# Kernel tuning notes

Hardware: AMD Instinct MI355X
Metric: run time of the kernel (lower is better)

The kernel has to match this reference:

```python
import jax, jax.numpy as jnp
import numpy as np


def setup_inputs() -> dict:
    key = jax.random.key(0)
    k1, k2 = jax.random.split(key)
    N, C, H, W = 2, 128, 256, 256
    k, m = 7, 8
    feat = jax.random.normal(k1, (N, C, H, W), dtype=jnp.float32)
    filters_lr = jax.random.normal(k2, (N, C * k * k, H // m, W // m), dtype=jnp.float32)
    return {"feat": feat, "filters_lr": filters_lr, "kernel_size": k, "block_size": m}


def _block_fac(feat, filters_lr, k, m):
    # feat: [N,C,H,W]; filters_lr: [N, C*k^2, H/m, W/m]
    N, C, H, W = feat.shape
    Hb, Wb = H // m, W // m
    k2 = k * k
    pad = (k - 1) // 2
    # weight_permute_reshape: NCHW -> NHWC -> [N,Hb,Wb,C,k2] (C slowest, then tap)
    w = jnp.transpose(filters_lr, (0, 2, 3, 1)).reshape(N, Hb, Wb, C, k2)
    x = jnp.transpose(feat, (0, 2, 3, 1))  # NHWC
    xp = jnp.pad(x, ((0, 0), (pad, pad), (pad, pad), (0, 0)))
    out = jnp.zeros_like(x)
    # tap index t = dh*k + dw (matches torch unfold(2,k) then unfold(3,k) ordering)
    for t in range(k2):
        dh, dw = t // k, t % k
        # per-block weight for this tap, upsampled to full resolution: [N,H,W,C]
        w_t = jnp.repeat(jnp.repeat(w[..., t], m, axis=1), m, axis=2)
        out = out + xp[:, dh:dh + H, dw:dw + W, :] * w_t
    return jnp.transpose(out, (0, 3, 1, 2))  # back to NCHW


def reference(feat, filters_lr, kernel_size, block_size):
    return _block_fac(feat, filters_lr, kernel_size, block_size)
```

## Files before the change

kernel.cpp:

```cpp
#include <hip/hip_runtime.h>
#include <stdint.h>


#define LDW   264
#define NROWS 14

typedef const uint32_t __attribute__((address_space(1))) guint;
typedef uint32_t __attribute__((address_space(3))) luint;

__global__ __launch_bounds__(64, 2)
void block_fac_kernel(const float* __restrict__ feat,
                      const float* __restrict__ filt,
                      float* __restrict__ out) {
    __shared__ float s_in[NROWS * LDW];

    const int bid = blockIdx.x;
    const int hb  = bid & 31;
    const int c   = (bid >> 5) & 127;
    const int n   = bid >> 12;
    const int lane = threadIdx.x;

    const int c0 = lane << 2;
    const int wb = lane >> 1;

    const float* wgbase = filt + (size_t)((n * 128 + c) * 49) * 1024 + hb * 32 + wb;
    float wt[49];
    #pragma unroll
    for (int t = 0; t < 49; ++t) wt[t] = wgbase[(size_t)t * 1024];

    const int H0 = hb * 8;
    const int h0 = H0 - 3;

    for (int idx = lane; idx < NROWS * 6; idx += 64) {
        int r = idx / 6, j = idx - r * 6;
        int p = (j < 3) ? (1 + j) : (257 + j);
        s_in[r * LDW + p] = 0.f;
    }

    const float* fbase = feat + (size_t)(n * 128 + c) * (256 * 256);
    #pragma unroll
    for (int r = 0; r < NROWS; ++r) {
        int gr = h0 + r;
        float* lp = &s_in[r * LDW + 4];
        if (gr >= 0 && gr < 256) {
            const float* gp = fbase + (size_t)gr * 256 + (lane << 2);
            __builtin_amdgcn_global_load_lds((guint*)gp, (luint*)lp, 16, 0, 0);
        } else {
            *(float4*)(&s_in[r * LDW + 4 + (lane << 2)]) =
                make_float4(0.f, 0.f, 0.f, 0.f);
        }
    }
    asm volatile("s_waitcnt vmcnt(0)" ::: "memory");

    float acc[8][4] = {};

    #pragma unroll
    for (int jj = 0; jj < NROWS; ++jj) {
        const float* rp = &s_in[jj * LDW + c0];
        float4 a0 = *(const float4*)(rp);
        float4 a1 = *(const float4*)(rp + 4);
        float4 a2 = *(const float4*)(rp + 8);
        float win[12] = {a0.x, a0.y, a0.z, a0.w,
                         a1.x, a1.y, a1.z, a1.w,
                         a2.x, a2.y, a2.z, a2.w};
        #pragma unroll
        for (int a = 0; a < 8; ++a) {
            int dh = jj - a;
            if (dh >= 0 && dh <= 6) {
                #pragma unroll
                for (int dw = 0; dw < 7; ++dw) {
                    float wv = wt[dh * 7 + dw];
                    #pragma unroll
                    for (int i = 0; i < 4; ++i)
                        acc[a][i] += win[i + dw + 1] * wv;
                }
            }
        }
    }

    float* obase = out + (size_t)((n * 128 + c) * 256 + H0) * 256 + c0;
    #pragma unroll
    for (int a = 0; a < 8; ++a)
        *(float4*)(obase + (size_t)(a * 256)) =
            make_float4(acc[a][0], acc[a][1], acc[a][2], acc[a][3]);
}

extern "C" void kernel_launch(void* const* d_in, const int* in_sizes, int n_in,
                              void* d_out, int out_size, void* d_ws, size_t ws_size,
                              hipStream_t stream) {
    const float* feat = (const float*)d_in[0];
    const float* filt = (const float*)d_in[1];
    float* out = (float*)d_out;
    dim3 grid(2 * 128 * 32);
    dim3 block(64);
    hipLaunchKernelGGL(block_fac_kernel, grid, block, 0, stream, feat, filt, out);
}
```

Baseline: 43.62 us.

## Replace LDS staging with direct register row loads and cross-lane bpermute halos

Drops the shared-memory tile and async global-to-LDS copy. Each lane now loads its 14 float4 rows straight into registers with clamped row indices, zeroing out-of-range rows. Horizontal neighbours come from ds_bpermute between adjacent lanes, with edge lanes masked to zero. This removes LDS allocation and the extra LDS reads, but it raises register pressure (launch bounds lowered to 1 wave per EU hint) and adds six bpermute ops per row.

New measurement: 41.24 us. 5.4% less time.

```diff
diff --git a/kernel.cpp b/kernel.cpp
--- a/kernel.cpp
+++ b/kernel.cpp
@@ -1,19 +1,10 @@
 #include <hip/hip_runtime.h>
-#include <stdint.h>
 
 
-#define LDW   264
-#define NROWS 14
-
-typedef const uint32_t __attribute__((address_space(1))) guint;
-typedef uint32_t __attribute__((address_space(3))) luint;
-
-__global__ __launch_bounds__(64, 2)
+__global__ __launch_bounds__(64, 1)
 void block_fac_kernel(const float* __restrict__ feat,
                       const float* __restrict__ filt,
                       float* __restrict__ out) {
-    __shared__ float s_in[NROWS * LDW];
-
     const int bid = blockIdx.x;
     const int hb  = bid & 31;
     const int c   = (bid >> 5) & 127;
@@ -22,47 +13,48 @@
 
     const int c0 = lane << 2;
     const int wb = lane >> 1;
+    const int H0 = hb * 8;
 
+    const float* fbase  = feat + (size_t)(n * 128 + c) * (256 * 256);
     const float* wgbase = filt + (size_t)((n * 128 + c) * 49) * 1024 + hb * 32 + wb;
+
+    float4 row[14];
+    #pragma unroll
+    for (int r = 0; r < 14; ++r) {
+        int gr  = H0 - 3 + r;
+        int grc = gr < 0 ? 0 : (gr > 255 ? 255 : gr);
+        row[r] = *(const float4*)(fbase + (size_t)grc * 256 + c0);
+    }
+
     float wt[49];
     #pragma unroll
     for (int t = 0; t < 49; ++t) wt[t] = wgbase[(size_t)t * 1024];
 
-    const int H0 = hb * 8;
-    const int h0 = H0 - 3;
-
-    for (int idx = lane; idx < NROWS * 6; idx += 64) {
-        int r = idx / 6, j = idx - r * 6;
-        int p = (j < 3) ? (1 + j) : (257 + j);
-        s_in[r * LDW + p] = 0.f;
-    }
-
-    const float* fbase = feat + (size_t)(n * 128 + c) * (256 * 256);
-    #pragma unroll
-    for (int r = 0; r < NROWS; ++r) {
-        int gr = h0 + r;
-        float* lp = &s_in[r * LDW + 4];
-        if (gr >= 0 && gr < 256) {
-            const float* gp = fbase + (size_t)gr * 256 + (lane << 2);
-            __builtin_amdgcn_global_load_lds((guint*)gp, (luint*)lp, 16, 0, 0);
-        } else {
-            *(float4*)(&s_in[r * LDW + 4 + (lane << 2)]) =
-                make_float4(0.f, 0.f, 0.f, 0.f);
-        }
-    }
-    asm volatile("s_waitcnt vmcnt(0)" ::: "memory");
+    const int addrL = ((lane - 1) & 63) << 2;
+    const int addrR = ((lane + 1) & 63) << 2;
+    const bool l0  = (lane == 0);
+    const bool l63 = (lane == 63);
 
     float acc[8][4] = {};
 
     #pragma unroll
-    for (int jj = 0; jj < NROWS; ++jj) {
-        const float* rp = &s_in[jj * LDW + c0];
-        float4 a0 = *(const float4*)(rp);
-        float4 a1 = *(const float4*)(rp + 4);
-        float4 a2 = *(const float4*)(rp + 8);
-        float win[12] = {a0.x, a0.y, a0.z, a0.w,
-                         a1.x, a1.y, a1.z, a1.w,
-                         a2.x, a2.y, a2.z, a2.w};
+    for (int jj = 0; jj < 14; ++jj) {
+        const int gr = H0 - 3 + jj;
+        float4 f = row[jj];
+        if (gr < 0 || gr > 255) f = make_float4(0.f, 0.f, 0.f, 0.f);
+
+        float L1 = __int_as_float(__builtin_amdgcn_ds_bpermute(addrL, __float_as_int(f.y)));
+        float L2 = __int_as_float(__builtin_amdgcn_ds_bpermute(addrL, __float_as_int(f.z)));
+        float L3 = __int_as_float(__builtin_amdgcn_ds_bpermute(addrL, __float_as_int(f.w)));
+        float R0 = __int_as_float(__builtin_amdgcn_ds_bpermute(addrR, __float_as_int(f.x)));
+        float R1 = __int_as_float(__builtin_amdgcn_ds_bpermute(addrR, __float_as_int(f.y)));
+        float R2 = __int_as_float(__builtin_amdgcn_ds_bpermute(addrR, __float_as_int(f.z)));
+        if (l0)  { L1 = 0.f; L2 = 0.f; L3 = 0.f; }
+        if (l63) { R0 = 0.f; R1 = 0.f; R2 = 0.f; }
+
+        float win[12] = {0.f, L1, L2, L3,
+                         f.x, f.y, f.z, f.w,
+                         R0, R1, R2, 0.f};
         #pragma unroll
         for (int a = 0; a < 8; ++a) {
             int dh = jj - a;
```
